# Kernel tuning notes

Measured on AMD Instinct MI355X. Metric: run time of the kernel, lower is better.

## Reference

```python
import jax, jax.numpy as jnp
import numpy as np

H, W, C = 200, 200, 256      # backbone feature map (stride-16)
N_ROI = 4096                 # proposals in the mini-batch
POOL = 7                     # RoI pool output size
G = 2                        # sampling grid per bin (2x2 -> max pooled)
HID = 256                    # FC head width
NCLS = 21                    # Pascal VOC classes incl. background


def setup_inputs() -> dict:
    key = jax.random.key(0)
    ks = jax.random.split(key, 10)
    features = jax.random.normal(ks[0], (H, W, C), jnp.float32)
    rois = jax.random.uniform(ks[1], (N_ROI, 4), jnp.float32)          # normalized (y1,x1,y2,x2), unordered
    labels = jax.random.randint(ks[2], (N_ROI,), 0, NCLS, jnp.int32)
    bbox_targets = jax.random.normal(ks[3], (N_ROI, 4), jnp.float32) * 0.1
    feat_dim = POOL * POOL * C
    W1 = jax.random.normal(ks[4], (feat_dim, HID), jnp.float32) * 0.01
    b1 = jnp.zeros((HID,), jnp.float32)
    Wc = jax.random.normal(ks[5], (HID, NCLS), jnp.float32) * 0.01
    bc = jnp.zeros((NCLS,), jnp.float32)
    Wb = jax.random.normal(ks[6], (HID, NCLS * 4), jnp.float32) * 0.01
    bb = jnp.zeros((NCLS * 4,), jnp.float32)
    return dict(features=features, rois=rois, labels=labels, bbox_targets=bbox_targets,
                W1=W1, b1=b1, Wc=Wc, bc=bc, Wb=Wb, bb=bb)


def _roi_pool(features, rois):
    # Batched RoI max-pool: sample a (POOL*G)x(POOL*G) nearest-neighbor grid per ROI,
    # then max over each GxG window -> [N, POOL, POOL, C].
    n = rois.shape[0]
    y1 = jnp.minimum(rois[:, 0], rois[:, 2]); y2 = jnp.maximum(rois[:, 0], rois[:, 2])
    x1 = jnp.minimum(rois[:, 1], rois[:, 3]); x2 = jnp.maximum(rois[:, 1], rois[:, 3])
    sp = POOL * G
    t = (jnp.arange(sp, dtype=jnp.float32) + 0.5) / sp                 # bin sample centers in [0,1)
    ys = y1[:, None] + (y2 - y1)[:, None] * t[None, :]                 # [N, sp]
    xs = x1[:, None] + (x2 - x1)[:, None] * t[None, :]
    iy = jnp.clip(jnp.round(ys * (H - 1)), 0, H - 1).astype(jnp.int32)
    ix = jnp.clip(jnp.round(xs * (W - 1)), 0, W - 1).astype(jnp.int32)
    g = features[iy[:, :, None], ix[:, None, :]]                       # [N, sp, sp, C] gather
    return g.reshape(n, POOL, G, POOL, G, C).max(axis=(2, 4))


def reference(features, rois, labels, bbox_targets, W1, b1, Wc, bc, Wb, bb):
    n = rois.shape[0]
    pooled = _roi_pool(features, rois)                                 # [N,7,7,C]
    x = pooled.reshape(n, -1)
    h = jax.nn.relu(x @ W1 + b1)                                       # [N,HID]
    cls_logits = h @ Wc + bc                                           # [N,NCLS]
    bbox_pred = (h @ Wb + bb).reshape(n, NCLS, 4)                      # class-specific deltas
    # classification loss: mean cross-entropy over ROIs
    logp = jax.nn.log_softmax(cls_logits, axis=-1)
    cls_loss = -jnp.mean(jnp.take_along_axis(logp, labels[:, None], axis=1))
    sel = jnp.take_along_axis(bbox_pred, labels[:, None, None], axis=1)[:, 0]  # [N,4]
    d = sel - bbox_targets
    ad = jnp.abs(d)
    sl1 = jnp.where(ad < 1.0, 0.5 * d * d, ad - 0.5)
    reg_loss = jnp.mean(jnp.sum(sl1, axis=-1))
    return cls_loss + reg_loss
```

## Files before the change

### kernel.cpp

```cpp
#include <hip/hip_runtime.h>

#define H_    200
#define W_    200
#define C_    256
#define NROI  4096
#define KDIM  12544
#define HID_  256
#define NCLS_ 21
#define NTASK (NROI * 49)
#define NSPLIT 8
#define NHEAD 112

typedef __bf16 bf16x8 __attribute__((ext_vector_type(8)));
typedef float  f32x4  __attribute__((ext_vector_type(4)));
typedef unsigned short u16x8 __attribute__((ext_vector_type(8)));

__device__ __forceinline__ unsigned short f2bf(float f) {
  unsigned u = __float_as_uint(f);
  return (unsigned short)((u + 0x7FFFu + ((u >> 16) & 1u)) >> 16);
}
__device__ __forceinline__ float bf2f(unsigned short u) {
  return __uint_as_float(((unsigned)u) << 16);
}
__device__ __forceinline__ void gload16(const void* g, void* l) {
  __builtin_amdgcn_global_load_lds((const __attribute__((address_space(1))) unsigned int*)g,
                                   (__attribute__((address_space(3))) unsigned int*)l, 16, 0, 0);
}

#define NB_CVT   2048
#define NB_TRN   3136
#define NB_WPR   112
#define NB_BAS   784

__global__ __launch_bounds__(256) void prep_all(
    const float* __restrict__ F, unsigned short* __restrict__ Fb,
    const float* __restrict__ W1, unsigned short* __restrict__ BT,
    const float* __restrict__ Wc, const float* __restrict__ bc,
    const float* __restrict__ Wb, const float* __restrict__ bb,
    unsigned short* __restrict__ WT, float* __restrict__ Wbias,
    const float* __restrict__ rois, short4* __restrict__ Bases) {
  __shared__ float tile[32][33];
  const int b = blockIdx.x;
  const int tid = threadIdx.x;

  if (b < NB_CVT) {
    const int n4 = (H_ * W_ * C_) / 4;
    for (int i = b * 256 + tid; i < n4; i += NB_CVT * 256) {
      float4 v = ((const float4*)F)[i];
      ushort4 o;
      o.x = f2bf(v.x); o.y = f2bf(v.y); o.z = f2bf(v.z); o.w = f2bf(v.w);
      ((ushort4*)Fb)[i] = o;
    }
  } else if (b < NB_CVT + NB_TRN) {
    const int id = b - NB_CVT;
    const int k0 = (id % 392) * 32;
    const int n0 = (id / 392) * 32;
    const int tx = tid & 31;
    const int ty = tid >> 5;
#pragma unroll
    for (int i = 0; i < 4; ++i)
      tile[ty + 8 * i][tx] = W1[(size_t)(k0 + ty + 8 * i) * HID_ + n0 + tx];
    __syncthreads();
#pragma unroll
    for (int i = 0; i < 4; ++i) {
      const int n = ty + 8 * i;
      BT[(size_t)(n0 + n) * KDIM + k0 + tx] = f2bf(tile[tx][n]);
    }
  } else if (b < NB_CVT + NB_TRN + NB_WPR) {
    const int n = b - (NB_CVT + NB_TRN);
    const int k = tid;
    float v = 0.f;
    if (n < 21)       v = Wc[(size_t)k * NCLS_ + n];
    else if (n < 105) v = Wb[(size_t)k * (NCLS_ * 4) + (n - 21)];
    WT[(size_t)n * HID_ + k] = f2bf(v);
    if (k == 0) Wbias[n] = (n < 21) ? bc[n] : ((n < 105) ? bb[n - 21] : 0.f);
  } else {
    const int task = (b - (NB_CVT + NB_TRN + NB_WPR)) * 256 + tid;
    const int roi  = task / 49;
    const int cell = task - roi * 49;
    const int py = cell / 7;
    const int px = cell - py * 7;

    float4 r = ((const float4*)rois)[roi];
    const float y1 = fminf(r.x, r.z), y2 = fmaxf(r.x, r.z);
    const float x1 = fminf(r.y, r.w), x2 = fmaxf(r.y, r.w);
    const float dy = __fsub_rn(y2, y1), dx = __fsub_rn(x2, x1);

    short v[4];
#pragma unroll
    for (int g = 0; g < 2; ++g) {
      float tyv = __fdiv_rn(__fadd_rn((float)(2 * py + g), 0.5f), 14.0f);
      float txv = __fdiv_rn(__fadd_rn((float)(2 * px + g), 0.5f), 14.0f);
      float ys = __fadd_rn(y1, __fmul_rn(dy, tyv));
      float xs = __fadd_rn(x1, __fmul_rn(dx, txv));
      int yi = (int)rintf(__fmul_rn(ys, 199.0f));
      int xi = (int)rintf(__fmul_rn(xs, 199.0f));
      v[g]     = (short)min(max(yi, 0), H_ - 1);
      v[2 + g] = (short)min(max(xi, 0), W_ - 1);
    }
    Bases[task] = make_short4(v[0], v[1], v[2], v[3]);
  }
}

__global__ __launch_bounds__(512) void gemm_fused(
    const unsigned short* __restrict__ Fb, const short4* __restrict__ Bases,
    const unsigned short* __restrict__ BT, unsigned short* __restrict__ Hp) {
  __shared__ __align__(16) unsigned char As[2][64 * 128];
  __shared__ __align__(16) unsigned char Bs[2][256 * 128];
  const int tid  = threadIdx.x;
  const int lane = tid & 63;
  const int wi   = tid >> 6;
  const int wr   = wi >> 2, wc = wi & 3;

  const int split = blockIdx.x & 7;
  const int bm    = blockIdx.x >> 3;
  const int c0 = (49 * split) >> 3;
  const int c1 = (49 * (split + 1)) >> 3;
  const int t0k = c0 * 4;
  const int nt  = (c1 - c0) * 4;

  const int rl = tid >> 3;
  const int g8 = tid & 7;
  const short4* bp = Bases + (size_t)(bm * 64 + rl) * 49;
  const int awb = rl * 128 + ((g8 * 16) ^ ((rl & 7) << 4));
  const unsigned short* fbg = Fb + g8 * 8;

  const unsigned short *p00, *p01, *p10, *p11;
#define SETPTRS(bv)                                        \
  p00 = fbg + ((size_t)((bv).x * W_ + (bv).z) * C_);       \
  p01 = fbg + ((size_t)((bv).x * W_ + (bv).w) * C_);       \
  p10 = fbg + ((size_t)((bv).y * W_ + (bv).z) * C_);       \
  p11 = fbg + ((size_t)((bv).y * W_ + (bv).w) * C_)

  const int srow  = lane >> 3;
  const int sbyte = ((lane & 7) << 4) ^ (srow << 4);
  const size_t kbase = (size_t)t0k * 64 + (sbyte >> 1);
  const unsigned short* gB[4];
  int lBo[4];
#pragma unroll
  for (int r = 0; r < 4; ++r) {
    const int row = r * 64 + wi * 8;
    gB[r]  = BT + (size_t)(row + srow) * KDIM + kbase;
    lBo[r] = row * 128;
  }

  int aoff[2][2], boff[4][2];
#pragma unroll
  for (int kf = 0; kf < 2; ++kf) {
    const int kb = kf * 64 + ((lane >> 4) << 4);
#pragma unroll
    for (int m = 0; m < 2; ++m) {
      const int arow = wr * 32 + m * 16 + (lane & 15);
      aoff[m][kf] = arow * 128 + (kb ^ ((arow & 7) << 4));
    }
#pragma unroll
    for (int n = 0; n < 4; ++n) {
      const int brow = wc * 64 + n * 16 + (lane & 15);
      boff[n][kf] = brow * 128 + (kb ^ ((brow & 7) << 4));
    }
  }

  f32x4 acc[2][4] = {};

  short4 nb = bp[c0];
  SETPTRS(nb);
  {
    const int pfc = (c0 + 1 < 49) ? c0 + 1 : 48;
    nb = bp[pfc];
  }
  {
    u16x8 a0 = *(const u16x8*)p00, a1 = *(const u16x8*)p01;
    u16x8 a2 = *(const u16x8*)p10, a3 = *(const u16x8*)p11;
    u16x8 o0;
#pragma unroll
    for (int j = 0; j < 8; ++j) {
      float m0 = fmaxf(fmaxf(bf2f(a0[j]), bf2f(a1[j])), fmaxf(bf2f(a2[j]), bf2f(a3[j])));
      o0[j] = (unsigned short)(__float_as_uint(m0) >> 16);
    }
    *(u16x8*)(&As[0][awb]) = o0;
#pragma unroll
    for (int r = 0; r < 4; ++r) gload16(gB[r], &Bs[0][lBo[r]]);
  }

  for (int t = 0; t < nt; ++t) {
    const int cur = t & 1;
    __syncthreads();

    const int pre = (t + 1 < nt);
    u16x8 a0, a1, a2, a3;
    if (pre) {
      const int tn = t + 1;
      const int qn = tn & 3;
      if (qn == 0) {
        SETPTRS(nb);
        const int cnx = c0 + (tn >> 2) + 1;
        const int pfc = (cnx < 49) ? cnx : 48;
        nb = bp[pfc];
      }
      const int qo = qn * 64;
      a0 = *(const u16x8*)(p00 + qo); a1 = *(const u16x8*)(p01 + qo);
      a2 = *(const u16x8*)(p10 + qo); a3 = *(const u16x8*)(p11 + qo);
      const size_t koff = (size_t)(t + 1) * 64;
      const int nx = cur ^ 1;
#pragma unroll
      for (int r = 0; r < 4; ++r) gload16(gB[r] + koff, &Bs[nx][lBo[r]]);
    }

    const unsigned char* Ab = As[cur];
    const unsigned char* Bb = Bs[cur];
#pragma unroll
    for (int kf = 0; kf < 2; ++kf) {
      bf16x8 af[2], bf[4];
#pragma unroll
      for (int m = 0; m < 2; ++m) af[m] = *(const bf16x8*)(Ab + aoff[m][kf]);
#pragma unroll
      for (int n = 0; n < 4; ++n) bf[n] = *(const bf16x8*)(Bb + boff[n][kf]);
#pragma unroll
      for (int m = 0; m < 2; ++m)
#pragma unroll
        for (int n = 0; n < 4; ++n)
          acc[m][n] = __builtin_amdgcn_mfma_f32_16x16x32_bf16(af[m], bf[n], acc[m][n], 0, 0, 0);
    }

    if (pre) {
      u16x8 o0;
#pragma unroll
      for (int j = 0; j < 8; ++j) {
        float m0 = fmaxf(fmaxf(bf2f(a0[j]), bf2f(a1[j])), fmaxf(bf2f(a2[j]), bf2f(a3[j])));
        o0[j] = (unsigned short)(__float_as_uint(m0) >> 16);
      }
      *(u16x8*)(&As[cur ^ 1][awb]) = o0;
    }
  }

  const int growb = bm * 64 + wr * 32 + ((lane >> 4) << 2);
  const int gcolb = wc * 64 + (lane & 15);
  unsigned short* Ho = Hp + (size_t)split * NROI * HID_;
#pragma unroll
  for (int m = 0; m < 2; ++m)
#pragma unroll
    for (int n = 0; n < 4; ++n)
#pragma unroll
      for (int j = 0; j < 4; ++j)
        Ho[(size_t)(growb + m * 16 + j) * HID_ + gcolb + n * 16] = f2bf(acc[m][n][j]);
}

__global__ __launch_bounds__(256) void head_loss(
    const unsigned short* __restrict__ Hp, const float* __restrict__ b1,
    const unsigned short* __restrict__ WT, const float* __restrict__ Wbias,
    const int* __restrict__ labels, const float* __restrict__ tgt,
    float* __restrict__ out) {
  __shared__ __align__(16) unsigned char A_lds[64 * 512];
  __shared__ float O_lds[64][113];
  const int tid = threadIdx.x;
  const int roiBase = blockIdx.x * 64;

  {
    const int rl  = tid >> 2;
    const int seg = tid & 3;
    const size_t rowoff = (size_t)(roiBase + rl) * HID_;
#pragma unroll
    for (int g = 0; g < 8; ++g) {
      const int chunk = g * 4 + seg;
      const int ch = chunk * 8;
      float s[8];
#pragma unroll
      for (int j = 0; j < 8; ++j) s[j] = b1[ch + j];
#pragma unroll
      for (int sp = 0; sp < NSPLIT; ++sp) {
        u16x8 v = *(const u16x8*)(Hp + (size_t)sp * NROI * HID_ + rowoff + ch);
#pragma unroll
        for (int j = 0; j < 8; ++j) s[j] += bf2f(v[j]);
      }
      u16x8 o;
#pragma unroll
      for (int j = 0; j < 8; ++j) o[j] = f2bf(fmaxf(s[j], 0.f));
      const int cb = chunk * 16;
      *(u16x8*)(&A_lds[rl * 512 + (cb ^ ((rl & 7) << 4))]) = o;
    }
  }
  __syncthreads();

  const int lane = tid & 63, w = tid >> 6;
  f32x4 acc[7] = {};
#pragma unroll
  for (int kf = 0; kf < 8; ++kf) {
    const int kb = kf * 64 + ((lane >> 4) << 4);
    const int arow = w * 16 + (lane & 15);
    bf16x8 av = *(const bf16x8*)(&A_lds[arow * 512 + (kb ^ ((arow & 7) << 4))]);
#pragma unroll
    for (int n = 0; n < 7; ++n) {
      bf16x8 bv = *(const bf16x8*)(WT + (size_t)(n * 16 + (lane & 15)) * HID_ + (kb >> 1));
      acc[n] = __builtin_amdgcn_mfma_f32_16x16x32_bf16(av, bv, acc[n], 0, 0, 0);
    }
  }
  {
    const int orow = w * 16 + ((lane >> 4) << 2);
#pragma unroll
    for (int n = 0; n < 7; ++n) {
      const int col = n * 16 + (lane & 15);
      const float bv = Wbias[col];
#pragma unroll
      for (int j = 0; j < 4; ++j) O_lds[orow + j][col] = acc[n][j] + bv;
    }
  }
  __syncthreads();

  if (tid < 64) {
    const int roi = roiBase + tid;
    const float* lg = O_lds[tid];
    float m = lg[0];
#pragma unroll
    for (int i = 1; i < NCLS_; ++i) m = fmaxf(m, lg[i]);
    float s = 0.f;
#pragma unroll
    for (int i = 0; i < NCLS_; ++i) s += expf(lg[i] - m);
    const float lse = m + logf(s);
    const int lab = labels[roi];
    float contrib = lse - lg[lab];
#pragma unroll
    for (int j = 0; j < 4; ++j) {
      float d = lg[NCLS_ + lab * 4 + j] - tgt[roi * 4 + j];
      float ad = fabsf(d);
      contrib += (ad < 1.f) ? 0.5f * d * d : ad - 0.5f;
    }
    contrib *= (1.0f / NROI);
#pragma unroll
    for (int off = 32; off > 0; off >>= 1) contrib += __shfl_down(contrib, off);
    if (tid == 0) atomicAdd(out, contrib);
  }
}

extern "C" void kernel_launch(void* const* d_in, const int* in_sizes, int n_in,
                              void* d_out, int out_size, void* d_ws, size_t ws_size,
                              hipStream_t stream) {
  const float* features = (const float*)d_in[0];
  const float* rois     = (const float*)d_in[1];
  const int*   labels   = (const int*)d_in[2];
  const float* tgt      = (const float*)d_in[3];
  const float* W1       = (const float*)d_in[4];
  const float* b1       = (const float*)d_in[5];
  const float* Wc       = (const float*)d_in[6];
  const float* bc       = (const float*)d_in[7];
  const float* Wb       = (const float*)d_in[8];
  const float* bb       = (const float*)d_in[9];

  char* ws = (char*)d_ws;
  unsigned short* Fb    = (unsigned short*)(ws);
  unsigned short* BTm   = (unsigned short*)(ws + 20480000);
  short4*         Bases = (short4*)(ws + 26902528);
  unsigned short* Hp    = (unsigned short*)(ws + 28508160);
  unsigned short* WT    = (unsigned short*)(ws + 45285376);
  float*          Wbias = (float*)(ws + 45342720);

  hipMemsetAsync(d_out, 0, (size_t)out_size * sizeof(float), stream);

  hipLaunchKernelGGL(prep_all, dim3(NB_CVT + NB_TRN + NB_WPR + NB_BAS), dim3(256), 0, stream,
                     features, Fb, W1, BTm, Wc, bc, Wb, bb, WT, Wbias, rois, Bases);
  hipLaunchKernelGGL(gemm_fused, dim3(512), dim3(512), 0, stream, Fb, Bases, BTm, Hp);
  hipLaunchKernelGGL(head_loss, dim3(NROI / 64), dim3(256), 0, stream,
                     Hp, b1, WT, Wbias, labels, tgt, (float*)d_out);
}
```

Before: 177.3 us.

## Shrink head_loss tiles to 16 ROIs per block, splitting N tiles across waves

The head_loss kernel now handles 16 ROIs per block instead of 64, so it launches four times as many blocks (256 instead of 64) to fill more of the GPU's compute units. Within a block, each of the four waves computes one or two 16-column output tiles for the shared 16-row A tile, instead of each wave owning 16 rows and all seven column tiles. LDS use drops accordingly. In exchange there are four times as many atomicAdds to the output, and the WT weights are re-read by more blocks.

```diff
diff --git a/kernel.cpp b/kernel.cpp
--- a/kernel.cpp
+++ b/kernel.cpp
@@ -250,63 +250,66 @@
     const unsigned short* __restrict__ WT, const float* __restrict__ Wbias,
     const int* __restrict__ labels, const float* __restrict__ tgt,
     float* __restrict__ out) {
-  __shared__ __align__(16) unsigned char A_lds[64 * 512];
-  __shared__ float O_lds[64][113];
+  __shared__ __align__(16) unsigned char A_lds[16 * 512];
+  __shared__ float O_lds[16][113];
   const int tid = threadIdx.x;
-  const int roiBase = blockIdx.x * 64;
-
-  {
-    const int rl  = tid >> 2;
-    const int seg = tid & 3;
-    const size_t rowoff = (size_t)(roiBase + rl) * HID_;
-#pragma unroll
-    for (int g = 0; g < 8; ++g) {
-      const int chunk = g * 4 + seg;
-      const int ch = chunk * 8;
-      float s[8];
-#pragma unroll
-      for (int j = 0; j < 8; ++j) s[j] = b1[ch + j];
-#pragma unroll
-      for (int sp = 0; sp < NSPLIT; ++sp) {
-        u16x8 v = *(const u16x8*)(Hp + (size_t)sp * NROI * HID_ + rowoff + ch);
-#pragma unroll
-        for (int j = 0; j < 8; ++j) s[j] += bf2f(v[j]);
-      }
-      u16x8 o;
-#pragma unroll
-      for (int j = 0; j < 8; ++j) o[j] = f2bf(fmaxf(s[j], 0.f));
-      const int cb = chunk * 16;
-      *(u16x8*)(&A_lds[rl * 512 + (cb ^ ((rl & 7) << 4))]) = o;
-    }
+  const int roiBase = blockIdx.x * 16;
+
+#pragma unroll
+  for (int s = 0; s < 2; ++s) {
+    const int slot  = tid + s * 256;
+    const int rl    = slot >> 5;
+    const int chunk = slot & 31;
+    const int ch    = chunk * 8;
+    const size_t rowoff = (size_t)(roiBase + rl) * HID_ + ch;
+    float sum[8];
+#pragma unroll
+    for (int j = 0; j < 8; ++j) sum[j] = b1[ch + j];
+#pragma unroll
+    for (int sp = 0; sp < NSPLIT; ++sp) {
+      u16x8 v = *(const u16x8*)(Hp + (size_t)sp * NROI * HID_ + rowoff);
+#pragma unroll
+      for (int j = 0; j < 8; ++j) sum[j] += bf2f(v[j]);
+    }
+    u16x8 o;
+#pragma unroll
+    for (int j = 0; j < 8; ++j) o[j] = f2bf(fmaxf(sum[j], 0.f));
+    const int cb = chunk * 16;
+    *(u16x8*)(&A_lds[rl * 512 + (cb ^ ((rl & 7) << 4))]) = o;
   }
   __syncthreads();
 
   const int lane = tid & 63, w = tid >> 6;
-  f32x4 acc[7] = {};
+  const int arow = lane & 15;
+  f32x4 acc0 = {}, acc1 = {};
+  const int n0t = w, n1t = w + 4;
+  const bool has2 = (n1t < 7);
 #pragma unroll
   for (int kf = 0; kf < 8; ++kf) {
     const int kb = kf * 64 + ((lane >> 4) << 4);
-    const int arow = w * 16 + (lane & 15);
     bf16x8 av = *(const bf16x8*)(&A_lds[arow * 512 + (kb ^ ((arow & 7) << 4))]);
-#pragma unroll
-    for (int n = 0; n < 7; ++n) {
-      bf16x8 bv = *(const bf16x8*)(WT + (size_t)(n * 16 + (lane & 15)) * HID_ + (kb >> 1));
-      acc[n] = __builtin_amdgcn_mfma_f32_16x16x32_bf16(av, bv, acc[n], 0, 0, 0);
+    bf16x8 bv0 = *(const bf16x8*)(WT + (size_t)(n0t * 16 + arow) * HID_ + (kb >> 1));
+    acc0 = __builtin_amdgcn_mfma_f32_16x16x32_bf16(av, bv0, acc0, 0, 0, 0);
+    if (has2) {
+      bf16x8 bv1 = *(const bf16x8*)(WT + (size_t)(n1t * 16 + arow) * HID_ + (kb >> 1));
+      acc1 = __builtin_amdgcn_mfma_f32_16x16x32_bf16(av, bv1, acc1, 0, 0, 0);
     }
   }
   {
-    const int orow = w * 16 + ((lane >> 4) << 2);
-#pragma unroll
-    for (int n = 0; n < 7; ++n) {
-      const int col = n * 16 + (lane & 15);
-      const float bv = Wbias[col];
-#pragma unroll
-      for (int j = 0; j < 4; ++j) O_lds[orow + j][col] = acc[n][j] + bv;
+    const int orow = (lane >> 4) << 2;
+#pragma unroll
+    for (int j = 0; j < 4; ++j) {
+      const int col0 = n0t * 16 + arow;
+      O_lds[orow + j][col0] = acc0[j] + Wbias[col0];
+      if (has2) {
+        const int col1 = n1t * 16 + arow;
+        O_lds[orow + j][col1] = acc1[j] + Wbias[col1];
+      }
     }
   }
   __syncthreads();
 
-  if (tid < 64) {
+  if (tid < 16) {
     const int roi = roiBase + tid;
     const float* lg = O_lds[tid];
     float m = lg[0];
@@ -325,8 +328,10 @@
       contrib += (ad < 1.f) ? 0.5f * d * d : ad - 0.5f;
     }
     contrib *= (1.0f / NROI);
-#pragma unroll
-    for (int off = 32; off > 0; off >>= 1) contrib += __shfl_down(contrib, off);
+    contrib += __shfl_down(contrib, 8);
+    contrib += __shfl_down(contrib, 4);
+    contrib += __shfl_down(contrib, 2);
+    contrib += __shfl_down(contrib, 1);
     if (tid == 0) atomicAdd(out, contrib);
   }
 }
@@ -358,6 +363,6 @@
   hipLaunchKernelGGL(prep_all, dim3(NB_CVT + NB_TRN + NB_WPR + NB_BAS), dim3(256), 0, stream,
                      features, Fb, W1, BTm, Wc, bc, Wb, bb, WT, Wbias, rois, Bases);
   hipLaunchKernelGGL(gemm_fused, dim3(512), dim3(512), 0, stream, Fb, Bases, BTm, Hp);
-  hipLaunchKernelGGL(head_loss, dim3(NROI / 64), dim3(256), 0, stream,
+  hipLaunchKernelGGL(head_loss, dim3(NROI / 16), dim3(256), 0, stream,
                      Hp, b1, WT, Wbias, labels, tgt, (float*)d_out);
 }
```

After: 172.1 us. -2.9%, faster.
